# Kernel optimization log

Measured on AMD Instinct MI355X. Metric: run time of the kernel, lower is better.

## Reference

```python
import jax, jax.numpy as jnp
import numpy as np

N, IN, OUT, E, S = 65536, 512, 512, 8, 64


def setup_inputs() -> dict:
    key = jax.random.key(0)
    k1, k2, k3, k4, k5 = jax.random.split(key, 5)
    bound = float(np.sqrt(1.0 / IN))
    x = jax.random.normal(k1, (N, IN), dtype=jnp.float32)
    expert_coefficients = jax.random.normal(k2, (S, E), dtype=jnp.float32)
    batch_indices = jax.random.randint(k3, (N,), 0, S)
    weights = jax.random.uniform(k4, (E, OUT, IN), dtype=jnp.float32, minval=-bound, maxval=bound)
    bias = jax.random.uniform(k5, (OUT,), dtype=jnp.float32, minval=-bound, maxval=bound)
    return {"x": x, "expert_coefficients": expert_coefficients,
            "batch_indices": batch_indices, "weights": weights, "bias": bias}


def reference(x, expert_coefficients, batch_indices, weights, bias):
    # Original computes mixed_weights[b] = sum_e coeff[b,e] * W[e], then for each
    # system b applies mixed_weights[b] to the atoms with batch_indices == b via a
    # masked scan. Linearity lets us equivalently gather per-atom expert
    # coefficients and contract once, avoiding the O(num_systems * N) waste:
    #   out[n,o] = sum_e coeff[batch_indices[n], e] * sum_i W[e,o,i] * x[n,i]
    coeff_per_atom = expert_coefficients[batch_indices]  # [N, E]
    out = jnp.einsum('ni,eoi,ne->no', x, weights, coeff_per_atom)  # [N, OUT]
    return out + bias
```

## Files before the change

kernel.cpp:

```cpp
#include <hip/hip_runtime.h>
#include <hip/hip_bf16.h>

#define NA   65536
#define DIN  512
#define DOUT 512
#define NE   8
#define NS   64
#define CAP  2048
#define BM   128
#define BN   128
#define BK   32

typedef __attribute__((ext_vector_type(8))) __bf16 bf16x8;
typedef __attribute__((ext_vector_type(4))) __bf16 bf16x4;
typedef __attribute__((ext_vector_type(4))) float floatx4;

__device__ __forceinline__ void async_load16(const void* g, void* l) {
  __builtin_amdgcn_global_load_lds(
      (__attribute__((address_space(1))) void*)(void*)g,
      (__attribute__((address_space(3))) void*)l,
      16, 0, 0);
}

__global__ void init_kernel(int* cursors) {
  int t = threadIdx.x;
  if (t < NS) cursors[t] = t * CAP;
}

__global__ void scatter_kernel(const int* __restrict__ bidx,
                               int* __restrict__ cursors,
                               int* __restrict__ perm) {
  __shared__ int hist[NS];
  __shared__ int base[NS];
  int t = threadIdx.x;
  if (t < NS) hist[t] = 0;
  __syncthreads();
  int n = blockIdx.x * 256 + t;
  int s = bidx[n];
  int rank = atomicAdd(&hist[s], 1);
  __syncthreads();
  if (t < NS && hist[t] > 0) base[t] = atomicAdd(&cursors[t], hist[t]);
  __syncthreads();
  perm[base[s] + rank] = n;
}

__global__ void mixw_kernel(const float* __restrict__ W,
                            const float* __restrict__ coeff,
                            ushort* __restrict__ mixedW) {
  int t = threadIdx.x;
  int base = blockIdx.x * 2048 + t * 8;
  float w[NE][8];
#pragma unroll
  for (int e = 0; e < NE; e++) {
    const float4* p = (const float4*)(W + e * (DOUT * DIN) + base);
    float4 a = p[0], b = p[1];
    w[e][0] = a.x; w[e][1] = a.y; w[e][2] = a.z; w[e][3] = a.w;
    w[e][4] = b.x; w[e][5] = b.y; w[e][6] = b.z; w[e][7] = b.w;
  }
  int s0 = blockIdx.y * 32;
  for (int si = 0; si < 32; si++) {
    int s = s0 + si;
    float o[8] = {0, 0, 0, 0, 0, 0, 0, 0};
#pragma unroll
    for (int e = 0; e < NE; e++) {
      float c = coeff[s * NE + e];
#pragma unroll
      for (int j = 0; j < 8; j++) o[j] += c * w[e][j];
    }
    union { bf16x8 v; uint4 u; } cv;
#pragma unroll
    for (int j = 0; j < 8; j++) cv.v[j] = (__bf16)o[j];
    *(uint4*)(mixedW + (size_t)s * (DOUT * DIN) + base) = cv.u;
  }
}

__global__ __launch_bounds__(256) void gemm_kernel(
    const float* __restrict__ x, const ushort* __restrict__ mixedW,
    const int* __restrict__ perm, const int* __restrict__ cursors,
    const float* __restrict__ bias, float* __restrict__ out) {
  int st = blockIdx.y;
  int s = st >> 4;
  int tt = st & 15;
  int count = cursors[s] - s * CAP;
  int r0 = tt * BM;
  if (r0 >= count) return;
  int rows = min(BM, count - r0);
  int n0 = blockIdx.x * BN;

  __shared__ __align__(16) ushort Alds[BM * BK];
  __shared__ __align__(16) ushort Blds[BN * BK];
  __shared__ int prow[BM];

  int tid = threadIdx.x;
  int lane = tid & 63;
  int wave = tid >> 6;

  if (tid < BM) prow[tid] = perm[s * CAP + r0 + min(tid, rows - 1)];
  __syncthreads();

  int chunk = tid & 7;
  const float* aptr[4];
#pragma unroll
  for (int q = 0; q < 4; q++) {
    int row = q * 32 + (tid >> 3);
    aptr[q] = x + (size_t)prow[row] * DIN + chunk * 4;
  }
  const ushort* bptr[2];
  ushort* bl[2];
#pragma unroll
  for (int j = 0; j < 2; j++) {
    int region = j * 4 + wave;
    int row = region * 16 + (lane >> 2);
    bptr[j] = mixedW + (size_t)s * (DOUT * DIN) + (size_t)(n0 + row) * DIN +
              (lane & 3) * 8;
    bl[j] = Blds + region * 512;
  }

  floatx4 acc[4][4];
#pragma unroll
  for (int mt = 0; mt < 4; mt++)
#pragma unroll
    for (int nt = 0; nt < 4; nt++) acc[mt][nt] = {0.f, 0.f, 0.f, 0.f};

  int wm = wave >> 1, wn = wave & 1;
  int m15 = lane & 15, quad = lane >> 4;

  for (int kk = 0; kk < DIN; kk += BK) {
#pragma unroll
    for (int j = 0; j < 2; j++) async_load16(bptr[j] + kk, bl[j]);
#pragma unroll
    for (int q = 0; q < 4; q++) {
      float4 v = *(const float4*)(aptr[q] + kk);
      bf16x4 h;
      h[0] = (__bf16)v.x; h[1] = (__bf16)v.y;
      h[2] = (__bf16)v.z; h[3] = (__bf16)v.w;
      int row = q * 32 + (tid >> 3);
      *(bf16x4*)(Alds + row * BK + chunk * 4) = h;
    }
    __syncthreads();
    bf16x8 af[4], bfm[4];
#pragma unroll
    for (int i = 0; i < 4; i++) {
      af[i]  = *(const bf16x8*)(Alds + (wm * 64 + i * 16 + m15) * BK + quad * 8);
      bfm[i] = *(const bf16x8*)(Blds + (wn * 64 + i * 16 + m15) * BK + quad * 8);
    }
#pragma unroll
    for (int mt = 0; mt < 4; mt++)
#pragma unroll
      for (int nt = 0; nt < 4; nt++)
        acc[mt][nt] = __builtin_amdgcn_mfma_f32_16x16x32_bf16(
            af[mt], bfm[nt], acc[mt][nt], 0, 0, 0);
    __syncthreads();
  }

  float bv[4];
#pragma unroll
  for (int nt = 0; nt < 4; nt++) bv[nt] = bias[n0 + wn * 64 + nt * 16 + m15];

#pragma unroll
  for (int mt = 0; mt < 4; mt++) {
    int rb = wm * 64 + mt * 16 + quad * 4;
    int pr[4];
#pragma unroll
    for (int r = 0; r < 4; r++) pr[r] = prow[rb + r];
#pragma unroll
    for (int nt = 0; nt < 4; nt++) {
      int col = n0 + wn * 64 + nt * 16 + m15;
#pragma unroll
      for (int r = 0; r < 4; r++) {
        if (rb + r < rows)
          out[(size_t)pr[r] * DOUT + col] = acc[mt][nt][r] + bv[nt];
      }
    }
  }
}

extern "C" void kernel_launch(void* const* d_in, const int* in_sizes, int n_in,
                              void* d_out, int out_size, void* d_ws,
                              size_t ws_size, hipStream_t stream) {
  const float* x     = (const float*)d_in[0];
  const float* coeff = (const float*)d_in[1];
  const int*   bidx  = (const int*)d_in[2];
  const float* W     = (const float*)d_in[3];
  const float* bias  = (const float*)d_in[4];
  float* out = (float*)d_out;

  char* ws = (char*)d_ws;
  int* cursors   = (int*)ws;
  int* perm      = (int*)(ws + 1024);
  ushort* mixedW = (ushort*)(ws + 1024 + CAP * NS * sizeof(int));

  hipLaunchKernelGGL(init_kernel, dim3(1), dim3(64), 0, stream, cursors);
  hipLaunchKernelGGL(scatter_kernel, dim3(NA / 256), dim3(256), 0, stream,
                     bidx, cursors, perm);
  hipLaunchKernelGGL(mixw_kernel, dim3(DOUT * DIN / 2048, 2), dim3(256), 0,
                     stream, W, coeff, mixedW);
  hipLaunchKernelGGL(gemm_kernel, dim3(DOUT / BN, NS * 16), dim3(256), 0,
                     stream, x, mixedW, perm, cursors, bias, out);
}
```

Measured before the change: 368.0 us.

## Pre-gather and convert activations to bf16 in a separate pass before GEMM

Adds a gather kernel that copies each atom's row of x, in permuted order, into a contiguous bf16 buffer. The GEMM can then load A tiles with async global-to-LDS copies, the same way it loads B, instead of doing per-row fp32 loads and conversions inside the k-loop. It also shrinks the per-system capacity so fewer empty tiles are launched, processes four atoms per thread in the scatter, and spreads mixw over more blocks. The cost is an extra pass over x and a bf16 staging buffer, and capacity 1280 relies on no system getting more than 1280 atoms.

```diff
diff --git a/kernel.cpp b/kernel.cpp
--- a/kernel.cpp
+++ b/kernel.cpp
@@ -6,13 +6,13 @@
 #define DOUT 512
 #define NE   8
 #define NS   64
-#define CAP  2048
+#define CAP  1280
 #define BM   128
 #define BN   128
 #define BK   32
+#define TPS  (CAP / BM)
 
 typedef __attribute__((ext_vector_type(8))) __bf16 bf16x8;
-typedef __attribute__((ext_vector_type(4))) __bf16 bf16x4;
 typedef __attribute__((ext_vector_type(4))) float floatx4;
 
 __device__ __forceinline__ void async_load16(const void* g, void* l) {
@@ -35,13 +35,39 @@
   int t = threadIdx.x;
   if (t < NS) hist[t] = 0;
   __syncthreads();
-  int n = blockIdx.x * 256 + t;
-  int s = bidx[n];
-  int rank = atomicAdd(&hist[s], 1);
+  int n0 = blockIdx.x * 1024;
+  int mys[4], myrank[4];
+#pragma unroll
+  for (int i = 0; i < 4; i++) {
+    mys[i] = bidx[n0 + i * 256 + t];
+    myrank[i] = atomicAdd(&hist[mys[i]], 1);
+  }
   __syncthreads();
   if (t < NS && hist[t] > 0) base[t] = atomicAdd(&cursors[t], hist[t]);
   __syncthreads();
-  perm[base[s] + rank] = n;
+#pragma unroll
+  for (int i = 0; i < 4; i++)
+    perm[base[mys[i]] + myrank[i]] = n0 + i * 256 + t;
+}
+
+__global__ void gather_kernel(const float* __restrict__ x,
+                              const int* __restrict__ perm,
+                              const int* __restrict__ cursors,
+                              ushort* __restrict__ xp) {
+  int rg = blockIdx.x * 4 + (threadIdx.x >> 6);
+  int lane = threadIdx.x & 63;
+  int s = rg / CAP;
+  int r = rg - s * CAP;
+  if (r >= cursors[s] - s * CAP) return;
+  int pr = perm[rg];
+  const float4* src = (const float4*)(x + (size_t)pr * DIN);
+  float4 a = src[2 * lane], b = src[2 * lane + 1];
+  union { bf16x8 v; uint4 u; } cv;
+  cv.v[0] = (__bf16)a.x; cv.v[1] = (__bf16)a.y;
+  cv.v[2] = (__bf16)a.z; cv.v[3] = (__bf16)a.w;
+  cv.v[4] = (__bf16)b.x; cv.v[5] = (__bf16)b.y;
+  cv.v[6] = (__bf16)b.z; cv.v[7] = (__bf16)b.w;
+  *(uint4*)(xp + (size_t)rg * DIN + lane * 8) = cv.u;
 }
 
 __global__ void mixw_kernel(const float* __restrict__ W,
@@ -57,8 +83,8 @@
     w[e][0] = a.x; w[e][1] = a.y; w[e][2] = a.z; w[e][3] = a.w;
     w[e][4] = b.x; w[e][5] = b.y; w[e][6] = b.z; w[e][7] = b.w;
   }
-  int s0 = blockIdx.y * 32;
-  for (int si = 0; si < 32; si++) {
+  int s0 = blockIdx.y * 8;
+  for (int si = 0; si < 8; si++) {
     int s = s0 + si;
     float o[8] = {0, 0, 0, 0, 0, 0, 0, 0};
 #pragma unroll
@@ -75,12 +101,12 @@
 }
 
 __global__ __launch_bounds__(256) void gemm_kernel(
-    const float* __restrict__ x, const ushort* __restrict__ mixedW,
+    const ushort* __restrict__ xp, const ushort* __restrict__ mixedW,
     const int* __restrict__ perm, const int* __restrict__ cursors,
     const float* __restrict__ bias, float* __restrict__ out) {
   int st = blockIdx.y;
-  int s = st >> 4;
-  int tt = st & 15;
+  int s = st / TPS;
+  int tt = st - s * TPS;
   int count = cursors[s] - s * CAP;
   int r0 = tt * BM;
   if (r0 >= count) return;
@@ -96,23 +122,19 @@
   int wave = tid >> 6;
 
   if (tid < BM) prow[tid] = perm[s * CAP + r0 + min(tid, rows - 1)];
-  __syncthreads();
-
-  int chunk = tid & 7;
-  const float* aptr[4];
-#pragma unroll
-  for (int q = 0; q < 4; q++) {
-    int row = q * 32 + (tid >> 3);
-    aptr[q] = x + (size_t)prow[row] * DIN + chunk * 4;
-  }
+
+  const ushort* aptr[2];
   const ushort* bptr[2];
+  ushort* al[2];
   ushort* bl[2];
 #pragma unroll
   for (int j = 0; j < 2; j++) {
     int region = j * 4 + wave;
     int row = region * 16 + (lane >> 2);
-    bptr[j] = mixedW + (size_t)s * (DOUT * DIN) + (size_t)(n0 + row) * DIN +
-              (lane & 3) * 8;
+    int kc = (lane & 3) * 8;
+    aptr[j] = xp + (size_t)(s * CAP + r0 + row) * DIN + kc;
+    bptr[j] = mixedW + (size_t)s * (DOUT * DIN) + (size_t)(n0 + row) * DIN + kc;
+    al[j] = Alds + region * 512;
     bl[j] = Blds + region * 512;
   }
 
@@ -127,15 +149,9 @@
 
   for (int kk = 0; kk < DIN; kk += BK) {
 #pragma unroll
-    for (int j = 0; j < 2; j++) async_load16(bptr[j] + kk, bl[j]);
-#pragma unroll
-    for (int q = 0; q < 4; q++) {
-      float4 v = *(const float4*)(aptr[q] + kk);
-      bf16x4 h;
-      h[0] = (__bf16)v.x; h[1] = (__bf16)v.y;
-      h[2] = (__bf16)v.z; h[3] = (__bf16)v.w;
-      int row = q * 32 + (tid >> 3);
-      *(bf16x4*)(Alds + row * BK + chunk * 4) = h;
+    for (int j = 0; j < 2; j++) {
+      async_load16(aptr[j] + kk, al[j]);
+      async_load16(bptr[j] + kk, bl[j]);
     }
     __syncthreads();
     bf16x8 af[4], bfm[4];
@@ -188,13 +204,17 @@
   char* ws = (char*)d_ws;
   int* cursors   = (int*)ws;
   int* perm      = (int*)(ws + 1024);
-  ushort* mixedW = (ushort*)(ws + 1024 + CAP * NS * sizeof(int));
+  ushort* mixedW = (ushort*)(ws + 1024 + NS * CAP * 4);
+  ushort* xp     = (ushort*)(ws + 1024 + NS * CAP * 4 +
+                             (size_t)NS * DOUT * DIN * 2);
 
   hipLaunchKernelGGL(init_kernel, dim3(1), dim3(64), 0, stream, cursors);
-  hipLaunchKernelGGL(scatter_kernel, dim3(NA / 256), dim3(256), 0, stream,
+  hipLaunchKernelGGL(scatter_kernel, dim3(NA / 1024), dim3(256), 0, stream,
                      bidx, cursors, perm);
-  hipLaunchKernelGGL(mixw_kernel, dim3(DOUT * DIN / 2048, 2), dim3(256), 0,
+  hipLaunchKernelGGL(gather_kernel, dim3(NS * CAP / 4), dim3(256), 0, stream,
+                     x, perm, cursors, xp);
+  hipLaunchKernelGGL(mixw_kernel, dim3(DOUT * DIN / 2048, 8), dim3(256), 0,
                      stream, W, coeff, mixedW);
-  hipLaunchKernelGGL(gemm_kernel, dim3(DOUT / BN, NS * 16), dim3(256), 0,
-                     stream, x, mixedW, perm, cursors, bias, out);
-}
+  hipLaunchKernelGGL(gemm_kernel, dim3(DOUT / BN, NS * TPS), dim3(256), 0,
+                     stream, xp, mixedW, perm, cursors, bias, out);
+}
```

After: 345.0 us. -6.3%, faster.
